# Kernel optimization log

Measured on AMD Instinct MI355X. Metric: run time of the kernel, lower is better.

Reference implementation:

```python
import jax, jax.numpy as jnp
import numpy as np

B, S, H = 4, 4096, 1024
I = 2048        # intermediate_size
E = 16          # num_experts
K = 2           # top_k


def setup_inputs() -> dict:
    key = jax.random.key(0)
    ks = jax.random.split(key, 5)
    scale = 0.02
    return {
        "hidden_states": jax.random.normal(ks[0], (B, S, H), dtype=jnp.float32),
        "w_gate": jax.random.normal(ks[1], (H, E), dtype=jnp.float32) * scale,
        "w_gate_proj": jax.random.normal(ks[2], (E, H, I), dtype=jnp.float32) * scale,
        "w_up_proj": jax.random.normal(ks[3], (E, H, I), dtype=jnp.float32) * scale,
        "w_down_proj": jax.random.normal(ks[4], (E, I, H), dtype=jnp.float32) * scale,
    }


def reference(hidden_states, w_gate, w_gate_proj, w_up_proj, w_down_proj):
    b, s, h = hidden_states.shape
    x = hidden_states.reshape(-1, h)                       # [T, H], T = b*s

    # --- gate: softmax router, top-k, renormalize (Mixtral-style) ---
    probs = jax.nn.softmax(x @ w_gate, axis=-1)            # [T, E]
    topk_vals, topk_idx = jax.lax.top_k(probs, K)          # [T, K]
    routing_weights = topk_vals / jnp.sum(topk_vals, axis=-1, keepdims=True)

    # --- per-expert SwiGLU FFN, combined via routing weights ---
    out = jnp.zeros_like(x)
    for e in range(E):
        # combined weight of expert e for each token (0 if not selected)
        we = jnp.sum(jnp.where(topk_idx == e, routing_weights, 0.0), axis=-1)  # [T]
        g = x @ w_gate_proj[e]                             # [T, I]
        u = x @ w_up_proj[e]                               # [T, I]
        y = (u * jax.nn.silu(g)) @ w_down_proj[e]          # [T, H]
        out = out + we[:, None] * y

    return out.reshape(b, s, h)
```

## Files before the change

### kernel.cpp

```cpp
#include <hip/hip_runtime.h>
#include <hip/hip_bf16.h>
#include <math.h>

#define T_TOK 16384
#define H_DIM 1024
#define I_DIM 2048
#define E_NUM 16
#define MAX_TILES 272

typedef short bf16x8 __attribute__((ext_vector_type(8)));
typedef float f32x4 __attribute__((ext_vector_type(4)));

static constexpr size_t XB_BYTES  = (size_t)T_TOK * H_DIM * 2;
static constexpr size_t W_BYTES   = (size_t)E_NUM * H_DIM * I_DIM * 2;
static constexpr size_t HB_BYTES  = (size_t)2 * T_TOK * I_DIM * 2;
static constexpr size_t LIST_BYTES= (size_t)E_NUM * T_TOK * 4;

static constexpr size_t XB_OFF    = 0;
static constexpr size_t WGT_OFF   = XB_OFF + XB_BYTES;
static constexpr size_t WUT_OFF   = WGT_OFF + W_BYTES;
static constexpr size_t WDT_OFF   = WUT_OFF + W_BYTES;
static constexpr size_t HB_OFF    = WDT_OFF + W_BYTES;
static constexpr size_t ROWS_OFF  = HB_OFF + HB_BYTES;
static constexpr size_t WTS_OFF   = ROWS_OFF + LIST_BYTES;
static constexpr size_t CNT_OFF   = WTS_OFF + LIST_BYTES;
static constexpr size_t BASE_OFF  = CNT_OFF + 256;
static constexpr size_t TILES_OFF = BASE_OFF + 256;
static constexpr size_t NT_OFF    = TILES_OFF + 2048;

__device__ __forceinline__ void async_ld16(void* lds, const void* g) {
    __builtin_amdgcn_global_load_lds(
        (const __attribute__((address_space(1))) void*)g,
        (__attribute__((address_space(3))) void*)lds,
        16, 0, 0);
}

__global__ void convert_x_kernel(const float* __restrict__ x, __hip_bfloat16* __restrict__ xb) {
    int i = (blockIdx.x * 256 + threadIdx.x) * 4;
    const float4 v = *(const float4*)(x + i);
    union { __hip_bfloat16 h[4]; ushort4 u; } cv;
    cv.h[0] = __float2bfloat16(v.x);
    cv.h[1] = __float2bfloat16(v.y);
    cv.h[2] = __float2bfloat16(v.z);
    cv.h[3] = __float2bfloat16(v.w);
    *(ushort4*)(xb + i) = cv.u;
}

__global__ void transpose_convert_kernel(const float* __restrict__ in,
                                         __hip_bfloat16* __restrict__ out,
                                         int R, int C) {
    __shared__ float tile[32][33];
    int e = blockIdx.z;
    int c0 = blockIdx.x * 32;
    int r0 = blockIdx.y * 32;
    const float* pin = in + (size_t)e * R * C;
    __hip_bfloat16* pout = out + (size_t)e * R * C;
    int tx = threadIdx.x, ty = threadIdx.y;
    #pragma unroll
    for (int j = 0; j < 4; j++)
        tile[ty + j*8][tx] = pin[(size_t)(r0 + ty + j*8) * C + (c0 + tx)];
    __syncthreads();
    #pragma unroll
    for (int j = 0; j < 4; j++)
        pout[(size_t)(c0 + ty + j*8) * R + (r0 + tx)] = __float2bfloat16(tile[tx][ty + j*8]);
}

__global__ void router_kernel(const float* __restrict__ x, const float* __restrict__ wg,
                              int* __restrict__ cnt, int* __restrict__ rows,
                              float* __restrict__ wts) {
    int t = blockIdx.x;
    int lane = threadIdx.x;
    float xv[16];
    const float* xp = x + (size_t)t * H_DIM;
    #pragma unroll
    for (int j = 0; j < 16; j++) xv[j] = xp[j*64 + lane];
    double logits[E_NUM];
    #pragma unroll
    for (int e = 0; e < E_NUM; e++) {
        double p = 0.0;
        #pragma unroll
        for (int j = 0; j < 16; j++)
            p += (double)xv[j] * (double)wg[(j*64 + lane) * E_NUM + e];
        #pragma unroll
        for (int off = 32; off > 0; off >>= 1) p += __shfl_down(p, off);
        logits[e] = p;
    }
    if (lane == 0) {
        int i1 = 0; double v1 = logits[0];
        #pragma unroll
        for (int e = 1; e < E_NUM; e++) if (logits[e] > v1) { v1 = logits[e]; i1 = e; }
        int i2 = -1; double v2 = -1e300;
        #pragma unroll
        for (int e = 0; e < E_NUM; e++) if (e != i1 && logits[e] > v2) { v2 = logits[e]; i2 = e; }
        double w1 = 1.0 / (1.0 + exp(v2 - v1));
        float w1f = (float)w1, w2f = (float)(1.0 - w1);
        int s1 = atomicAdd(&cnt[i1], 1);
        rows[i1 * T_TOK + s1] = t; wts[i1 * T_TOK + s1] = w1f;
        int s2 = atomicAdd(&cnt[i2], 1);
        rows[i2 * T_TOK + s2] = t; wts[i2 * T_TOK + s2] = w2f;
    }
}

__global__ void schedule_kernel(const int* __restrict__ cnt, int* __restrict__ base,
                                int* __restrict__ tiles, int* __restrict__ ntiles) {
    int b = 0, nt = 0;
    for (int e = 0; e < E_NUM; e++) {
        base[e] = b;
        int c = cnt[e];
        int m = (c + 127) >> 7;
        for (int i = 0; i < m; i++) tiles[nt++] = (e << 16) | i;
        b += c;
    }
    ntiles[0] = nt;
}

template<int MODE>
__global__ __launch_bounds__(256) void moe_gemm_kernel(
    const __hip_bfloat16* __restrict__ Abase,
    const __hip_bfloat16* __restrict__ Bw,
    void* __restrict__ Cout,
    const int* __restrict__ rows, const float* __restrict__ wts,
    const int* __restrict__ cnt, const int* __restrict__ base,
    const int* __restrict__ tiles, const int* __restrict__ ntiles,
    int Kd, int Nd)
{
    if ((int)blockIdx.y >= ntiles[0]) return;
    int td = tiles[blockIdx.y];
    int e = td >> 16, tile = td & 0xffff;
    int cnt_e = cnt[e], base_e = base[e];
    int cnt_local = cnt_e - tile * 128;
    int bn = blockIdx.x;
    const int* rows_e = rows + e * T_TOK;
    const __hip_bfloat16* Be = Bw + (size_t)e * Nd * Kd;

    __shared__ __align__(16) __hip_bfloat16 As[8][128][8];
    __shared__ __align__(16) __hip_bfloat16 Bs[8][128][8];

    int tid = threadIdx.x;
    int w = tid >> 6, lane = tid & 63;

    const __hip_bfloat16* aptr[4];
    const __hip_bfloat16* bptr[4];
    uint32_t loff[4];
    #pragma unroll
    for (int j = 0; j < 4; j++) {
        int u = w * 4 + j;
        int chunk = u >> 1, half = u & 1;
        int r = half * 64 + lane;
        int gr = tile * 128 + r;
        size_t arow;
        if (MODE == 2) {
            int rr = base_e + gr;
            if (rr > 2 * T_TOK - 1) rr = 2 * T_TOK - 1;
            arow = (size_t)rr;
        } else {
            arow = (size_t)((gr < cnt_e) ? rows_e[gr] : 0);
        }
        aptr[j] = Abase + arow * Kd + chunk * 8;
        bptr[j] = Be + (size_t)(bn * 128 + r) * Kd + chunk * 8;
        loff[j] = (uint32_t)(u * 1024);
    }

    int wm = w >> 1, wn = w & 1;
    int l16 = lane & 15, quad = lane >> 4;

    f32x4 acc[4][4];
    #pragma unroll
    for (int a = 0; a < 4; a++)
        #pragma unroll
        for (int b = 0; b < 4; b++) acc[a][b] = (f32x4){0.f, 0.f, 0.f, 0.f};

    char* AsB = (char*)&As[0][0][0];
    char* BsB = (char*)&Bs[0][0][0];

    for (int k0 = 0; k0 < Kd; k0 += 64) {
        #pragma unroll
        for (int j = 0; j < 4; j++) {
            async_ld16(AsB + loff[j], aptr[j]);
            async_ld16(BsB + loff[j], bptr[j]);
            aptr[j] += 64; bptr[j] += 64;
        }
        __syncthreads();
        #pragma unroll
        for (int ks = 0; ks < 2; ks++) {
            bf16x8 af[4], bfr[4];
            #pragma unroll
            for (int mt = 0; mt < 4; mt++)
                af[mt] = *(const bf16x8*)&As[ks*4 + quad][wm*64 + mt*16 + l16][0];
            #pragma unroll
            for (int nt = 0; nt < 4; nt++)
                bfr[nt] = *(const bf16x8*)&Bs[ks*4 + quad][wn*64 + nt*16 + l16][0];
            #pragma unroll
            for (int mt = 0; mt < 4; mt++)
                #pragma unroll
                for (int nt = 0; nt < 4; nt++)
                    acc[mt][nt] = __builtin_amdgcn_mfma_f32_16x16x32_bf16(af[mt], bfr[nt], acc[mt][nt], 0, 0, 0);
        }
        __syncthreads();
    }

    #pragma unroll
    for (int mt = 0; mt < 4; mt++) {
        #pragma unroll
        for (int r = 0; r < 4; r++) {
            int row = wm*64 + mt*16 + quad*4 + r;
            if (row < cnt_local) {
                int gr = tile * 128 + row;
                if (MODE == 0) {
                    __hip_bfloat16* hp = (__hip_bfloat16*)Cout + (size_t)(base_e + gr) * Nd;
                    #pragma unroll
                    for (int nt = 0; nt < 4; nt++) {
                        int col = bn*128 + wn*64 + nt*16 + l16;
                        hp[col] = __float2bfloat16(acc[mt][nt][r]);
                    }
                } else if (MODE == 1) {
                    __hip_bfloat16* hp = (__hip_bfloat16*)Cout + (size_t)(base_e + gr) * Nd;
                    #pragma unroll
                    for (int nt = 0; nt < 4; nt++) {
                        int col = bn*128 + wn*64 + nt*16 + l16;
                        float g = __bfloat162float(hp[col]);
                        float u = acc[mt][nt][r];
                        hp[col] = __float2bfloat16(u * (g / (1.f + expf(-g))));
                    }
                } else {
                    int token = rows_e[gr];
                    float wt = (wts + e * T_TOK)[gr];
                    float* op = (float*)Cout + (size_t)token * H_DIM + bn*128 + wn*64;
                    #pragma unroll
                    for (int nt = 0; nt < 4; nt++)
                        atomicAdd(op + nt*16 + l16, wt * acc[mt][nt][r]);
                }
            }
        }
    }
}

extern "C" void kernel_launch(void* const* d_in, const int* in_sizes, int n_in,
                              void* d_out, int out_size, void* d_ws, size_t ws_size,
                              hipStream_t stream) {
    const float* x   = (const float*)d_in[0];
    const float* wg  = (const float*)d_in[1];
    const float* wgp = (const float*)d_in[2];
    const float* wup = (const float*)d_in[3];
    const float* wdp = (const float*)d_in[4];
    float* out = (float*)d_out;
    char* ws = (char*)d_ws;

    __hip_bfloat16* xb   = (__hip_bfloat16*)(ws + XB_OFF);
    __hip_bfloat16* Wgt  = (__hip_bfloat16*)(ws + WGT_OFF);
    __hip_bfloat16* Wut  = (__hip_bfloat16*)(ws + WUT_OFF);
    __hip_bfloat16* Wdt  = (__hip_bfloat16*)(ws + WDT_OFF);
    __hip_bfloat16* hbuf = (__hip_bfloat16*)(ws + HB_OFF);
    int*   rowsp  = (int*)(ws + ROWS_OFF);
    float* wtsp   = (float*)(ws + WTS_OFF);
    int*   cntp   = (int*)(ws + CNT_OFF);
    int*   basep  = (int*)(ws + BASE_OFF);
    int*   tilesp = (int*)(ws + TILES_OFF);
    int*   ntp    = (int*)(ws + NT_OFF);

    hipMemsetAsync(cntp, 0, 256, stream);
    hipMemsetAsync(out, 0, (size_t)out_size * sizeof(float), stream);

    convert_x_kernel<<<(T_TOK * H_DIM) / 1024, 256, 0, stream>>>(x, xb);
    transpose_convert_kernel<<<dim3(I_DIM/32, H_DIM/32, E_NUM), dim3(32, 8), 0, stream>>>(wgp, Wgt, H_DIM, I_DIM);
    transpose_convert_kernel<<<dim3(I_DIM/32, H_DIM/32, E_NUM), dim3(32, 8), 0, stream>>>(wup, Wut, H_DIM, I_DIM);
    transpose_convert_kernel<<<dim3(H_DIM/32, I_DIM/32, E_NUM), dim3(32, 8), 0, stream>>>(wdp, Wdt, I_DIM, H_DIM);
    router_kernel<<<T_TOK, 64, 0, stream>>>(x, wg, cntp, rowsp, wtsp);
    schedule_kernel<<<1, 1, 0, stream>>>(cntp, basep, tilesp, ntp);

    moe_gemm_kernel<0><<<dim3(I_DIM/128, MAX_TILES), 256, 0, stream>>>(
        xb, Wgt, hbuf, rowsp, wtsp, cntp, basep, tilesp, ntp, H_DIM, I_DIM);
    moe_gemm_kernel<1><<<dim3(I_DIM/128, MAX_TILES), 256, 0, stream>>>(
        xb, Wut, hbuf, rowsp, wtsp, cntp, basep, tilesp, ntp, H_DIM, I_DIM);
    moe_gemm_kernel<2><<<dim3(H_DIM/128, MAX_TILES), 256, 0, stream>>>(
        hbuf, Wdt, out, rowsp, wtsp, cntp, basep, tilesp, ntp, I_DIM, H_DIM);
}
```

Baseline: 1.964 ms.

## Fuse gate/up GEMMs with interleaved weights, double-buffer LDS, fold x conversion into router

Gate and up projection weights are interleaved into one combined matrix in 16-column groups, so a single GEMM computes both and applies SiLU*up in the epilogue. This removes the second GEMM pass and the read-modify-write of the intermediate buffer. The GEMM main loop is now double-buffered in LDS so the next K-slice's async loads overlap with the MFMAs on the current one, which doubles shared memory use. The separate x-to-bf16 conversion kernel is folded into the router kernel, which already reads x.

```diff
diff --git a/kernel.cpp b/kernel.cpp
--- a/kernel.cpp
+++ b/kernel.cpp
@@ -12,15 +12,15 @@
 typedef float f32x4 __attribute__((ext_vector_type(4)));
 
 static constexpr size_t XB_BYTES  = (size_t)T_TOK * H_DIM * 2;
-static constexpr size_t W_BYTES   = (size_t)E_NUM * H_DIM * I_DIM * 2;
+static constexpr size_t WC_BYTES  = (size_t)E_NUM * 2 * I_DIM * H_DIM * 2;
+static constexpr size_t WD_BYTES  = (size_t)E_NUM * H_DIM * I_DIM * 2;
 static constexpr size_t HB_BYTES  = (size_t)2 * T_TOK * I_DIM * 2;
 static constexpr size_t LIST_BYTES= (size_t)E_NUM * T_TOK * 4;
 
 static constexpr size_t XB_OFF    = 0;
-static constexpr size_t WGT_OFF   = XB_OFF + XB_BYTES;
-static constexpr size_t WUT_OFF   = WGT_OFF + W_BYTES;
-static constexpr size_t WDT_OFF   = WUT_OFF + W_BYTES;
-static constexpr size_t HB_OFF    = WDT_OFF + W_BYTES;
+static constexpr size_t WC_OFF    = XB_OFF + XB_BYTES;
+static constexpr size_t WDT_OFF   = WC_OFF + WC_BYTES;
+static constexpr size_t HB_OFF    = WDT_OFF + WD_BYTES;
 static constexpr size_t ROWS_OFF  = HB_OFF + HB_BYTES;
 static constexpr size_t WTS_OFF   = ROWS_OFF + LIST_BYTES;
 static constexpr size_t CNT_OFF   = WTS_OFF + LIST_BYTES;
@@ -35,45 +35,40 @@
         16, 0, 0);
 }
 
-__global__ void convert_x_kernel(const float* __restrict__ x, __hip_bfloat16* __restrict__ xb) {
-    int i = (blockIdx.x * 256 + threadIdx.x) * 4;
-    const float4 v = *(const float4*)(x + i);
-    union { __hip_bfloat16 h[4]; ushort4 u; } cv;
-    cv.h[0] = __float2bfloat16(v.x);
-    cv.h[1] = __float2bfloat16(v.y);
-    cv.h[2] = __float2bfloat16(v.z);
-    cv.h[3] = __float2bfloat16(v.w);
-    *(ushort4*)(xb + i) = cv.u;
-}
-
 __global__ void transpose_convert_kernel(const float* __restrict__ in,
                                          __hip_bfloat16* __restrict__ out,
-                                         int R, int C) {
+                                         int R, int C, int Nd, int ioff) {
     __shared__ float tile[32][33];
     int e = blockIdx.z;
     int c0 = blockIdx.x * 32;
     int r0 = blockIdx.y * 32;
     const float* pin = in + (size_t)e * R * C;
-    __hip_bfloat16* pout = out + (size_t)e * R * C;
+    __hip_bfloat16* pout = out + (size_t)e * Nd * R;
     int tx = threadIdx.x, ty = threadIdx.y;
     #pragma unroll
     for (int j = 0; j < 4; j++)
         tile[ty + j*8][tx] = pin[(size_t)(r0 + ty + j*8) * C + (c0 + tx)];
     __syncthreads();
     #pragma unroll
-    for (int j = 0; j < 4; j++)
-        pout[(size_t)(c0 + ty + j*8) * R + (r0 + tx)] = __float2bfloat16(tile[tx][ty + j*8]);
+    for (int j = 0; j < 4; j++) {
+        int c = c0 + ty + j*8;
+        int n = (ioff < 0) ? c : 32*(c >> 4) + ioff + (c & 15);
+        pout[(size_t)n * R + (r0 + tx)] = __float2bfloat16(tile[tx][ty + j*8]);
+    }
 }
 
 __global__ void router_kernel(const float* __restrict__ x, const float* __restrict__ wg,
                               int* __restrict__ cnt, int* __restrict__ rows,
-                              float* __restrict__ wts) {
+                              float* __restrict__ wts, __hip_bfloat16* __restrict__ xb) {
     int t = blockIdx.x;
     int lane = threadIdx.x;
     float xv[16];
     const float* xp = x + (size_t)t * H_DIM;
+    __hip_bfloat16* xbp = xb + (size_t)t * H_DIM;
     #pragma unroll
     for (int j = 0; j < 16; j++) xv[j] = xp[j*64 + lane];
+    #pragma unroll
+    for (int j = 0; j < 16; j++) xbp[j*64 + lane] = __float2bfloat16(xv[j]);
     double logits[E_NUM];
     #pragma unroll
     for (int e = 0; e < E_NUM; e++) {
@@ -133,8 +128,8 @@
     const int* rows_e = rows + e * T_TOK;
     const __hip_bfloat16* Be = Bw + (size_t)e * Nd * Kd;
 
-    __shared__ __align__(16) __hip_bfloat16 As[8][128][8];
-    __shared__ __align__(16) __hip_bfloat16 Bs[8][128][8];
+    __shared__ __align__(16) __hip_bfloat16 As[2][8][128][8];
+    __shared__ __align__(16) __hip_bfloat16 Bs[2][8][128][8];
 
     int tid = threadIdx.x;
     int w = tid >> 6, lane = tid & 63;
@@ -170,26 +165,38 @@
         #pragma unroll
         for (int b = 0; b < 4; b++) acc[a][b] = (f32x4){0.f, 0.f, 0.f, 0.f};
 
-    char* AsB = (char*)&As[0][0][0];
-    char* BsB = (char*)&Bs[0][0][0];
-
-    for (int k0 = 0; k0 < Kd; k0 += 64) {
-        #pragma unroll
-        for (int j = 0; j < 4; j++) {
-            async_ld16(AsB + loff[j], aptr[j]);
-            async_ld16(BsB + loff[j], bptr[j]);
-            aptr[j] += 64; bptr[j] += 64;
-        }
-        __syncthreads();
+    char* AsB = (char*)&As[0][0][0][0];
+    char* BsB = (char*)&Bs[0][0][0][0];
+
+    #pragma unroll
+    for (int j = 0; j < 4; j++) {
+        async_ld16(AsB + loff[j], aptr[j]);
+        async_ld16(BsB + loff[j], bptr[j]);
+        aptr[j] += 64; bptr[j] += 64;
+    }
+    __syncthreads();
+
+    int nk = Kd >> 6;
+    int cur = 0;
+    for (int k0 = 0; k0 < nk; ++k0) {
+        if (k0 + 1 < nk) {
+            int nxt = cur ^ 1;
+            #pragma unroll
+            for (int j = 0; j < 4; j++) {
+                async_ld16(AsB + nxt * 16384 + loff[j], aptr[j]);
+                async_ld16(BsB + nxt * 16384 + loff[j], bptr[j]);
+                aptr[j] += 64; bptr[j] += 64;
+            }
+        }
         #pragma unroll
         for (int ks = 0; ks < 2; ks++) {
             bf16x8 af[4], bfr[4];
             #pragma unroll
             for (int mt = 0; mt < 4; mt++)
-                af[mt] = *(const bf16x8*)&As[ks*4 + quad][wm*64 + mt*16 + l16][0];
+                af[mt] = *(const bf16x8*)&As[cur][ks*4 + quad][wm*64 + mt*16 + l16][0];
             #pragma unroll
             for (int nt = 0; nt < 4; nt++)
-                bfr[nt] = *(const bf16x8*)&Bs[ks*4 + quad][wn*64 + nt*16 + l16][0];
+                bfr[nt] = *(const bf16x8*)&Bs[cur][ks*4 + quad][wn*64 + nt*16 + l16][0];
             #pragma unroll
             for (int mt = 0; mt < 4; mt++)
                 #pragma unroll
@@ -197,6 +204,7 @@
                     acc[mt][nt] = __builtin_amdgcn_mfma_f32_16x16x32_bf16(af[mt], bfr[nt], acc[mt][nt], 0, 0, 0);
         }
         __syncthreads();
+        cur ^= 1;
     }
 
     #pragma unroll
@@ -207,20 +215,13 @@
             if (row < cnt_local) {
                 int gr = tile * 128 + row;
                 if (MODE == 0) {
-                    __hip_bfloat16* hp = (__hip_bfloat16*)Cout + (size_t)(base_e + gr) * Nd;
+                    __hip_bfloat16* hp = (__hip_bfloat16*)Cout + (size_t)(base_e + gr) * I_DIM;
                     #pragma unroll
-                    for (int nt = 0; nt < 4; nt++) {
-                        int col = bn*128 + wn*64 + nt*16 + l16;
-                        hp[col] = __float2bfloat16(acc[mt][nt][r]);
-                    }
-                } else if (MODE == 1) {
-                    __hip_bfloat16* hp = (__hip_bfloat16*)Cout + (size_t)(base_e + gr) * Nd;
-                    #pragma unroll
-                    for (int nt = 0; nt < 4; nt++) {
-                        int col = bn*128 + wn*64 + nt*16 + l16;
-                        float g = __bfloat162float(hp[col]);
-                        float u = acc[mt][nt][r];
-                        hp[col] = __float2bfloat16(u * (g / (1.f + expf(-g))));
+                    for (int p = 0; p < 2; p++) {
+                        int icol = (bn*4 + wn*2 + p)*16 + l16;
+                        float g = acc[mt][2*p][r];
+                        float u = acc[mt][2*p+1][r];
+                        hp[icol] = __float2bfloat16(u * (g / (1.f + expf(-g))));
                     }
                 } else {
                     int token = rows_e[gr];
@@ -247,8 +248,7 @@
     char* ws = (char*)d_ws;
 
     __hip_bfloat16* xb   = (__hip_bfloat16*)(ws + XB_OFF);
-    __hip_bfloat16* Wgt  = (__hip_bfloat16*)(ws + WGT_OFF);
-    __hip_bfloat16* Wut  = (__hip_bfloat16*)(ws + WUT_OFF);
+    __hip_bfloat16* Wc   = (__hip_bfloat16*)(ws + WC_OFF);
     __hip_bfloat16* Wdt  = (__hip_bfloat16*)(ws + WDT_OFF);
     __hip_bfloat16* hbuf = (__hip_bfloat16*)(ws + HB_OFF);
     int*   rowsp  = (int*)(ws + ROWS_OFF);
@@ -261,17 +261,17 @@
     hipMemsetAsync(cntp, 0, 256, stream);
     hipMemsetAsync(out, 0, (size_t)out_size * sizeof(float), stream);
 
-    convert_x_kernel<<<(T_TOK * H_DIM) / 1024, 256, 0, stream>>>(x, xb);
-    transpose_convert_kernel<<<dim3(I_DIM/32, H_DIM/32, E_NUM), dim3(32, 8), 0, stream>>>(wgp, Wgt, H_DIM, I_DIM);
-    transpose_convert_kernel<<<dim3(I_DIM/32, H_DIM/32, E_NUM), dim3(32, 8), 0, stream>>>(wup, Wut, H_DIM, I_DIM);
-    transpose_convert_kernel<<<dim3(H_DIM/32, I_DIM/32, E_NUM), dim3(32, 8), 0, stream>>>(wdp, Wdt, I_DIM, H_DIM);
-    router_kernel<<<T_TOK, 64, 0, stream>>>(x, wg, cntp, rowsp, wtsp);
+    transpose_convert_kernel<<<dim3(I_DIM/32, H_DIM/32, E_NUM), dim3(32, 8), 0, stream>>>(
+        wgp, Wc, H_DIM, I_DIM, 2*I_DIM, 0);
+    transpose_convert_kernel<<<dim3(I_DIM/32, H_DIM/32, E_NUM), dim3(32, 8), 0, stream>>>(
+        wup, Wc, H_DIM, I_DIM, 2*I_DIM, 16);
+    transpose_convert_kernel<<<dim3(H_DIM/32, I_DIM/32, E_NUM), dim3(32, 8), 0, stream>>>(
+        wdp, Wdt, I_DIM, H_DIM, H_DIM, -1);
+    router_kernel<<<T_TOK, 64, 0, stream>>>(x, wg, cntp, rowsp, wtsp, xb);
     schedule_kernel<<<1, 1, 0, stream>>>(cntp, basep, tilesp, ntp);
 
-    moe_gemm_kernel<0><<<dim3(I_DIM/128, MAX_TILES), 256, 0, stream>>>(
-        xb, Wgt, hbuf, rowsp, wtsp, cntp, basep, tilesp, ntp, H_DIM, I_DIM);
-    moe_gemm_kernel<1><<<dim3(I_DIM/128, MAX_TILES), 256, 0, stream>>>(
-        xb, Wut, hbuf, rowsp, wtsp, cntp, basep, tilesp, ntp, H_DIM, I_DIM);
+    moe_gemm_kernel<0><<<dim3(2*I_DIM/128, MAX_TILES), 256, 0, stream>>>(
+        xb, Wc, hbuf, rowsp, wtsp, cntp, basep, tilesp, ntp, H_DIM, 2*I_DIM);
     moe_gemm_kernel<2><<<dim3(H_DIM/128, MAX_TILES), 256, 0, stream>>>(
         hbuf, Wdt, out, rowsp, wtsp, cntp, basep, tilesp, ntp, I_DIM, H_DIM);
 }
```

Result: faster. 1.876 ms (-4.5%).
